# Kernel optimization log

Hardware: AMD Instinct MI355X
Metric: run time of the kernel (lower is better)

## Reference

```python
import jax, jax.numpy as jnp
import numpy as np

B, N, D = 4, 4096, 512
H = 8
HD = D // H  # 64


def setup_inputs() -> dict:
    key = jax.random.key(0)
    ks = jax.random.split(key, 9)
    s = 1.0 / np.sqrt(D)
    return {
        "x": jax.random.normal(ks[0], (B, N, D), dtype=jnp.float32),
        "Wq": jax.random.normal(ks[1], (D, D), dtype=jnp.float32) * s,
        "bq": jax.random.normal(ks[2], (D,), dtype=jnp.float32) * 0.01,
        "Wk": jax.random.normal(ks[3], (D, D), dtype=jnp.float32) * s,
        "bk": jax.random.normal(ks[4], (D,), dtype=jnp.float32) * 0.01,
        "Wv": jax.random.normal(ks[5], (D, D), dtype=jnp.float32) * s,
        "bv": jax.random.normal(ks[6], (D,), dtype=jnp.float32) * 0.01,
        "Wo": jax.random.normal(ks[7], (D, D), dtype=jnp.float32) * s,
        "bo": jax.random.normal(ks[8], (D,), dtype=jnp.float32) * 0.01,
    }


def reference(x, Wq, bq, Wk, bk, Wv, bv, Wo, bo):
    # projections -> [B, H, N, HD]
    def split_heads(t):
        return t.reshape(B, N, H, HD).transpose(0, 2, 1, 3)

    q = split_heads(x @ Wq.T + bq)
    k = split_heads(x @ Wk.T + bk)
    v = split_heads(x @ Wv.T + bv)

    scale = 1.0 / np.sqrt(HD).astype(np.float32)
    scores = jnp.einsum("bhqd,bhkd->bhqk", q, k) * scale  # [B,H,N,N]
    attn = jax.nn.softmax(scores, axis=-1)
    out = jnp.einsum("bhqk,bhkd->bhqd", attn, v)  # [B,H,N,HD]
    out = out.transpose(0, 2, 1, 3).reshape(B, N, D)
    return out @ Wo.T + bo
```

## Files before the change

kernel.cpp:

```cpp
#include <hip/hip_runtime.h>
#include <hip/hip_bf16.h>

#define BB 4
#define NN 4096
#define DD 512
#define HH 8
#define HD 64

typedef __attribute__((ext_vector_type(4))) float f32x4;
typedef __attribute__((ext_vector_type(16))) float f32x16;
typedef __attribute__((ext_vector_type(8))) short short8;
typedef __attribute__((ext_vector_type(4))) unsigned int uint4v;

static __device__ __forceinline__ unsigned short f2bf(float f) {
    unsigned int u = __float_as_uint(f);
    u += 0x7fff + ((u >> 16) & 1);
    return (unsigned short)(u >> 16);
}

__global__ void convert_bf16(const float* __restrict__ in,
                             unsigned short* __restrict__ out, int n) {
    int i = (blockIdx.x * blockDim.x + threadIdx.x) * 8;
    int stride = gridDim.x * blockDim.x * 8;
    for (; i + 7 < n; i += stride) {
        f32x4 a = *reinterpret_cast<const f32x4*>(in + i);
        f32x4 b = *reinterpret_cast<const f32x4*>(in + i + 4);
        short8 o;
        o[0] = (short)f2bf(a[0]); o[1] = (short)f2bf(a[1]);
        o[2] = (short)f2bf(a[2]); o[3] = (short)f2bf(a[3]);
        o[4] = (short)f2bf(b[0]); o[5] = (short)f2bf(b[1]);
        o[6] = (short)f2bf(b[2]); o[7] = (short)f2bf(b[3]);
        *reinterpret_cast<short8*>(out + i) = o;
    }
}

__global__ void convert_weights(const float* __restrict__ W0, const float* __restrict__ W1,
                                const float* __restrict__ W2, const float* __restrict__ W3,
                                unsigned short* __restrict__ out) {
    int which = blockIdx.x >> 7;
    const float* src = which == 0 ? W0 : which == 1 ? W1 : which == 2 ? W2 : W3;
    unsigned short* dst = out + (size_t)which * DD * DD;
    int i = ((blockIdx.x & 127) * blockDim.x + threadIdx.x) * 8;
    f32x4 a = *reinterpret_cast<const f32x4*>(src + i);
    f32x4 b = *reinterpret_cast<const f32x4*>(src + i + 4);
    short8 o;
    o[0] = (short)f2bf(a[0]); o[1] = (short)f2bf(a[1]);
    o[2] = (short)f2bf(a[2]); o[3] = (short)f2bf(a[3]);
    o[4] = (short)f2bf(b[0]); o[5] = (short)f2bf(b[1]);
    o[6] = (short)f2bf(b[2]); o[7] = (short)f2bf(b[3]);
    *reinterpret_cast<short8*>(dst + i) = o;
}

template <int OUT_BF16>
__global__ __launch_bounds__(256)
void gemm_bias(const unsigned short* __restrict__ A,
               const unsigned short* __restrict__ W,
               const float* __restrict__ bias,
               void* __restrict__ Cout, float scale) {
    __shared__ uint4 ldsA[128 * 4];
    __shared__ uint4 ldsB[128 * 4];
    const int t = threadIdx.x;
    const int lane = t & 63;
    const int w = t >> 6;
    const int wr = w >> 1, wc = w & 1;
    const int brow = (int)blockIdx.y * 128;
    const int bcol = (int)blockIdx.x * 128;
    const int l16 = lane & 15;
    const int lq = lane >> 4;

    f32x4 acc[4][4] = {};

    const int sr = t >> 1;
    const int c16 = (t & 1) * 2;

    for (int k0 = 0; k0 < 512; k0 += 32) {
        const uint4* gA = reinterpret_cast<const uint4*>(A + (size_t)(brow + sr) * 512 + k0 + c16 * 8);
        const uint4* gB = reinterpret_cast<const uint4*>(W + (size_t)(bcol + sr) * 512 + k0 + c16 * 8);
        uint4 a0 = gA[0], a1 = gA[1];
        uint4 b0 = gB[0], b1 = gB[1];
        __syncthreads();
        ldsA[(sr * 4 + c16) ^ (sr & 7)]     = a0;
        ldsA[(sr * 4 + c16 + 1) ^ (sr & 7)] = a1;
        ldsB[(sr * 4 + c16) ^ (sr & 7)]     = b0;
        ldsB[(sr * 4 + c16 + 1) ^ (sr & 7)] = b1;
        __syncthreads();
        short8 af[4], bfr[4];
#pragma unroll
        for (int m = 0; m < 4; ++m) {
            int ra = wr * 64 + m * 16 + l16;
            af[m] = *reinterpret_cast<short8*>(&ldsA[(ra * 4 + lq) ^ (ra & 7)]);
            int rb = wc * 64 + m * 16 + l16;
            bfr[m] = *reinterpret_cast<short8*>(&ldsB[(rb * 4 + lq) ^ (rb & 7)]);
        }
#pragma unroll
        for (int m = 0; m < 4; ++m)
#pragma unroll
            for (int n = 0; n < 4; ++n)
                acc[m][n] = __builtin_amdgcn_mfma_f32_16x16x32_bf16(af[m], bfr[n], acc[m][n], 0, 0, 0);
    }

#pragma unroll
    for (int m = 0; m < 4; ++m) {
        int row = brow + wr * 64 + m * 16 + lq * 4;
#pragma unroll
        for (int n = 0; n < 4; ++n) {
            int col = bcol + wc * 64 + n * 16 + l16;
            float bv = bias[col];
#pragma unroll
            for (int r = 0; r < 4; ++r) {
                float v = (acc[m][n][r] + bv) * scale;
                if (OUT_BF16) {
                    ((unsigned short*)Cout)[(size_t)(row + r) * 512 + col] = f2bf(v);
                } else {
                    ((float*)Cout)[(size_t)(row + r) * 512 + col] = v;
                }
            }
        }
    }
}

__global__ __launch_bounds__(256)
void transpose_v(const unsigned short* __restrict__ Vb, unsigned short* __restrict__ Vt) {
    __shared__ unsigned short tile[64][72];
    const int bh = blockIdx.y;
    const int b = bh >> 3, h = bh & 7;
    const int n0 = blockIdx.x * 64;
    const int t = threadIdx.x;
    {
        int r = t >> 2;
        int cs = (t & 3) * 16;
        const short8* src = reinterpret_cast<const short8*>(
            Vb + (size_t)(b * NN + n0 + r) * DD + h * HD + cs);
        short8 v0 = src[0], v1 = src[1];
#pragma unroll
        for (int j = 0; j < 8; ++j) {
            tile[r][cs + j]     = (unsigned short)v0[j];
            tile[r][cs + 8 + j] = (unsigned short)v1[j];
        }
    }
    __syncthreads();
    {
        int d = t >> 2;
        int ns = (t & 3) * 16;
        short8 o0, o1;
#pragma unroll
        for (int j = 0; j < 8; ++j) {
            o0[j] = (short)tile[ns + j][d];
            o1[j] = (short)tile[ns + 8 + j][d];
        }
        unsigned short* dst = Vt + ((size_t)bh * HD + d) * NN + n0 + ns;
        *reinterpret_cast<short8*>(dst)     = o0;
        *reinterpret_cast<short8*>(dst + 8) = o1;
    }
}

__global__ __launch_bounds__(256)
void flash_attn(const unsigned short* __restrict__ Qb,
                const unsigned short* __restrict__ Kb,
                const unsigned short* __restrict__ Vt,
                unsigned short* __restrict__ Ob) {
    __shared__ __align__(16) char lds[32768];
    const int t = threadIdx.x;
    const int lane = t & 63;
    const int w = t >> 6;
    const int nid = (blockIdx.x & 7) * 128 + (blockIdx.x >> 3);
    const int bh = nid >> 5;
    const int qb = nid & 31;
    const int b = bh >> 3, h = bh & 7;
    const int q0 = qb * 128 + w * 32;
    const int l32 = lane & 31;
    const int hi = lane >> 5;

    const int i8 = lane >> 3, g8 = lane & 7;

    const unsigned short* qptr = Qb + (size_t)(b * NN + q0 + l32) * DD + h * HD + hi * 8;
    short8 qf[4];
#pragma unroll
    for (int c = 0; c < 4; ++c)
        qf[c] = *reinterpret_cast<const short8*>(qptr + c * 16);

    short8 ones;
#pragma unroll
    for (int j = 0; j < 8; ++j) ones[j] = (short)0x3F80;

    f32x16 OT0 = {}, OT1 = {}, OTS = {};

    auto STAGE = [&](int kvn, int bb) {
#pragma unroll
        for (int jj = 0; jj < 2; ++jj) {
            int rowl = w * 16 + jj * 8 + i8;
            int gsrc = (g8 ^ i8 ^ ((2 * w + jj) & 7)) * 8;
            const unsigned short* ks = Kb + (size_t)(b * NN + kvn + rowl) * DD + h * HD + gsrc;
            const unsigned short* vs = Vt + ((size_t)bh * HD + rowl) * NN + kvn + gsrc;
            __builtin_amdgcn_global_load_lds(
                (const __attribute__((address_space(1))) void*)ks,
                (__attribute__((address_space(3))) void*)(lds + bb + (w * 16 + jj * 8) * 128),
                16, 0, 0);
            __builtin_amdgcn_global_load_lds(
                (const __attribute__((address_space(1))) void*)vs,
                (__attribute__((address_space(3))) void*)(lds + bb + 8192 + (w * 16 + jj * 8) * 128),
                16, 0, 0);
        }
    };

    STAGE(0, 0);
    __syncthreads();

    int bufb = 0;
    for (int step = 0; step < NN / 64; ++step) {
        if (step < NN / 64 - 1) STAGE((step + 1) * 64, bufb ^ 16384);
        const char* Kt  = lds + bufb;
        const char* Vtl = lds + bufb + 8192;
#pragma unroll
        for (int sub = 0; sub < 2; ++sub) {
            short8 kf[4];
#pragma unroll
            for (int c = 0; c < 4; ++c) {
                int row = sub * 32 + l32;
                int g = (hi + 2 * c) ^ (row & 7) ^ ((row >> 3) & 7);
                kf[c] = *reinterpret_cast<const short8*>(Kt + row * 128 + (g << 4));
            }
            short8 vf[2][2];
#pragma unroll
            for (int dblk = 0; dblk < 2; ++dblk)
#pragma unroll
                for (int c2 = 0; c2 < 2; ++c2) {
                    int row = dblk * 32 + l32;
                    int g = ((sub << 2) + (c2 << 1) + hi) ^ (row & 7) ^ ((row >> 3) & 7);
                    vf[dblk][c2] = *reinterpret_cast<const short8*>(Vtl + row * 128 + (g << 4));
                }
            f32x16 S = {};
            __builtin_amdgcn_s_setprio(1);
            S = __builtin_amdgcn_mfma_f32_32x32x16_bf16(kf[0], qf[0], S, 0, 0, 0);
            S = __builtin_amdgcn_mfma_f32_32x32x16_bf16(kf[1], qf[1], S, 0, 0, 0);
            S = __builtin_amdgcn_mfma_f32_32x32x16_bf16(kf[2], qf[2], S, 0, 0, 0);
            S = __builtin_amdgcn_mfma_f32_32x32x16_bf16(kf[3], qf[3], S, 0, 0, 0);
            __builtin_amdgcn_s_setprio(0);

            unsigned int wq[8];
#pragma unroll
            for (int j = 0; j < 8; ++j) {
                float p0 = __builtin_exp2f(S[2 * j]);
                float p1 = __builtin_exp2f(S[2 * j + 1]);
                asm("v_cvt_pk_bf16_f32 %0, %1, %2" : "=v"(wq[j]) : "v"(p0), "v"(p1));
            }
            asm("v_permlane32_swap_b32 %0, %1" : "+v"(wq[0]), "+v"(wq[2]));
            asm("v_permlane32_swap_b32 %0, %1" : "+v"(wq[1]), "+v"(wq[3]));
            asm("v_permlane32_swap_b32 %0, %1" : "+v"(wq[4]), "+v"(wq[6]));
            asm("v_permlane32_swap_b32 %0, %1" : "+v"(wq[5]), "+v"(wq[7]));
            uint4v pu0 = {wq[0], wq[1], wq[2], wq[3]};
            uint4v pu1 = {wq[4], wq[5], wq[6], wq[7]};
            short8 pc0 = __builtin_bit_cast(short8, pu0);
            short8 pc1 = __builtin_bit_cast(short8, pu1);

            __builtin_amdgcn_s_setprio(1);
            OT0 = __builtin_amdgcn_mfma_f32_32x32x16_bf16(vf[0][0], pc0, OT0, 0, 0, 0);
            OT0 = __builtin_amdgcn_mfma_f32_32x32x16_bf16(vf[0][1], pc1, OT0, 0, 0, 0);
            OT1 = __builtin_amdgcn_mfma_f32_32x32x16_bf16(vf[1][0], pc0, OT1, 0, 0, 0);
            OT1 = __builtin_amdgcn_mfma_f32_32x32x16_bf16(vf[1][1], pc1, OT1, 0, 0, 0);
            OTS = __builtin_amdgcn_mfma_f32_32x32x16_bf16(ones,     pc0, OTS, 0, 0, 0);
            OTS = __builtin_amdgcn_mfma_f32_32x32x16_bf16(ones,     pc1, OTS, 0, 0, 0);
            __builtin_amdgcn_s_setprio(0);
        }
        __syncthreads();
        bufb ^= 16384;
    }

    float inv = 1.0f / OTS[0];
    char* lw = lds + w * 4096;
#pragma unroll
    for (int dblk = 0; dblk < 2; ++dblk) {
#pragma unroll
        for (int g = 0; g < 4; ++g) {
#pragma unroll
            for (int j = 0; j < 2; ++j) {
                int r = 4 * g + 2 * j;
                int d = dblk * 32 + 8 * g + 2 * j + 4 * hi;
                float a = (dblk ? OT1[r] : OT0[r]) * inv;
                float bqv = (dblk ? OT1[r + 1] : OT0[r + 1]) * inv;
                unsigned int wv;
                asm("v_cvt_pk_bf16_f32 %0, %1, %2" : "=v"(wv) : "v"(a), "v"(bqv));
                int addr = (l32 * 128 + d * 2) ^ ((l32 & 7) << 4);
                *reinterpret_cast<unsigned int*>(lw + addr) = wv;
            }
        }
    }
#pragma unroll
    for (int it = 0; it < 4; ++it) {
        int q = lane >> 1;
        int seg = (lane & 1) + it * 2;
        uint4 val = *reinterpret_cast<uint4*>(lw + ((q * 128 + seg * 16) ^ ((q & 7) << 4)));
        *reinterpret_cast<uint4*>(Ob + (size_t)(b * NN + q0 + q) * DD + h * HD + seg * 8) = val;
    }
}

extern "C" void kernel_launch(void* const* d_in, const int* in_sizes, int n_in,
                              void* d_out, int out_size, void* d_ws, size_t ws_size,
                              hipStream_t stream) {
    (void)in_sizes; (void)n_in; (void)out_size; (void)ws_size;
    const float* x  = (const float*)d_in[0];
    const float* Wq = (const float*)d_in[1];
    const float* bq = (const float*)d_in[2];
    const float* Wk = (const float*)d_in[3];
    const float* bk = (const float*)d_in[4];
    const float* Wv = (const float*)d_in[5];
    const float* bv = (const float*)d_in[6];
    const float* Wo = (const float*)d_in[7];
    const float* bo = (const float*)d_in[8];
    float* out = (float*)d_out;

    char* ws = (char*)d_ws;
    const size_t BUF = 16777216;
    unsigned short* xb  = (unsigned short*)(ws);
    unsigned short* Qb  = (unsigned short*)(ws + BUF);
    unsigned short* Kb  = (unsigned short*)(ws + 2 * BUF);
    unsigned short* Vb  = (unsigned short*)(ws + 3 * BUF);
    unsigned short* Wqb = (unsigned short*)(ws + 4 * BUF);
    unsigned short* Wkb = Wqb + 262144;
    unsigned short* Wvb = Wkb + 262144;
    unsigned short* Wob = Wvb + 262144;
    unsigned short* Vt  = xb;
    unsigned short* Ob  = Vb;

    const int NTOK = BB * NN;
    const float cl = 0.125f * 1.4426950408889634f;

    convert_bf16<<<2048, 256, 0, stream>>>(x, xb, NTOK * DD);
    convert_weights<<<512, 256, 0, stream>>>(Wq, Wk, Wv, Wo, Wqb);

    dim3 ggrid(4, NTOK / 128);
    gemm_bias<1><<<ggrid, 256, 0, stream>>>(xb, Wqb, bq, Qb, cl);
    gemm_bias<1><<<ggrid, 256, 0, stream>>>(xb, Wkb, bk, Kb, 1.0f);
    gemm_bias<1><<<ggrid, 256, 0, stream>>>(xb, Wvb, bv, Vb, 1.0f);

    transpose_v<<<dim3(NN / 64, BB * HH), 256, 0, stream>>>(Vb, Vt);

    flash_attn<<<1024, 256, 0, stream>>>(Qb, Kb, Vt, Ob);

    gemm_bias<0><<<ggrid, 256, 0, stream>>>(Ob, Wob, bo, out, 1.0f);
}
```

Measured before the change: 315.8 us.

## Restructure attention inner loop: precompute LDS offsets, interleave two S tiles

Precomputes the swizzled LDS read offsets and the global staging pointers once, and advances the pointers incrementally instead of recomputing addresses every step. The kv loop is unrolled by two so the double-buffer offsets become compile-time constants. Both 32-key S tiles are computed with interleaved MFMA chains, which gives independent MFMAs to hide dependency latency and overlaps the second softmax with PV MFMAs. The setprio hints are dropped, and the extra live fragments raise register pressure.

```diff
diff --git a/kernel.cpp b/kernel.cpp
--- a/kernel.cpp
+++ b/kernel.cpp
@@ -183,87 +183,118 @@
 #pragma unroll
     for (int j = 0; j < 8; ++j) ones[j] = (short)0x3F80;
 
+    const f32x16 Z = {};
     f32x16 OT0 = {}, OT1 = {}, OTS = {};
 
-    auto STAGE = [&](int kvn, int bb) {
-#pragma unroll
-        for (int jj = 0; jj < 2; ++jj) {
-            int rowl = w * 16 + jj * 8 + i8;
-            int gsrc = (g8 ^ i8 ^ ((2 * w + jj) & 7)) * 8;
-            const unsigned short* ks = Kb + (size_t)(b * NN + kvn + rowl) * DD + h * HD + gsrc;
-            const unsigned short* vs = Vt + ((size_t)bh * HD + rowl) * NN + kvn + gsrc;
-            __builtin_amdgcn_global_load_lds(
-                (const __attribute__((address_space(1))) void*)ks,
-                (__attribute__((address_space(3))) void*)(lds + bb + (w * 16 + jj * 8) * 128),
-                16, 0, 0);
-            __builtin_amdgcn_global_load_lds(
-                (const __attribute__((address_space(1))) void*)vs,
-                (__attribute__((address_space(3))) void*)(lds + bb + 8192 + (w * 16 + jj * 8) * 128),
-                16, 0, 0);
-        }
+    int koff[8], voff[8];
+#pragma unroll
+    for (int sub = 0; sub < 2; ++sub) {
+#pragma unroll
+        for (int c = 0; c < 4; ++c) {
+            int row = sub * 32 + l32;
+            int g = (hi + 2 * c) ^ (row & 7) ^ ((row >> 3) & 7);
+            koff[sub * 4 + c] = row * 128 + g * 16;
+        }
+#pragma unroll
+        for (int dblk = 0; dblk < 2; ++dblk)
+#pragma unroll
+            for (int c2 = 0; c2 < 2; ++c2) {
+                int row = dblk * 32 + l32;
+                int g = ((sub << 2) + (c2 << 1) + hi) ^ (row & 7) ^ ((row >> 3) & 7);
+                voff[sub * 4 + dblk * 2 + c2] = 8192 + row * 128 + g * 16;
+            }
+    }
+
+    const int rowl0 = w * 16 + i8;
+    const int rowl1 = w * 16 + 8 + i8;
+    const int gs0 = (g8 ^ i8 ^ ((2 * w) & 7)) * 8;
+    const int gs1 = (g8 ^ i8 ^ ((2 * w + 1) & 7)) * 8;
+    const unsigned short* kp0 = Kb + (size_t)(b * NN + rowl0) * DD + h * HD + gs0;
+    const unsigned short* kp1 = Kb + (size_t)(b * NN + rowl1) * DD + h * HD + gs1;
+    const unsigned short* vp0 = Vt + ((size_t)bh * HD + rowl0) * NN + gs0;
+    const unsigned short* vp1 = Vt + ((size_t)bh * HD + rowl1) * NN + gs1;
+
+    auto STAGE = [&](int bb) {
+        __builtin_amdgcn_global_load_lds(
+            (const __attribute__((address_space(1))) void*)kp0,
+            (__attribute__((address_space(3))) void*)(lds + bb + (w * 16) * 128), 16, 0, 0);
+        __builtin_amdgcn_global_load_lds(
+            (const __attribute__((address_space(1))) void*)kp1,
+            (__attribute__((address_space(3))) void*)(lds + bb + (w * 16 + 8) * 128), 16, 0, 0);
+        __builtin_amdgcn_global_load_lds(
+            (const __attribute__((address_space(1))) void*)vp0,
+            (__attribute__((address_space(3))) void*)(lds + bb + 8192 + (w * 16) * 128), 16, 0, 0);
+        __builtin_amdgcn_global_load_lds(
+            (const __attribute__((address_space(1))) void*)vp1,
+            (__attribute__((address_space(3))) void*)(lds + bb + 8192 + (w * 16 + 8) * 128), 16, 0, 0);
+        kp0 += 64 * DD; kp1 += 64 * DD; vp0 += 64; vp1 += 64;
     };
 
-    STAGE(0, 0);
+    auto softpack = [&](const f32x16& S, short8& pa, short8& pb) {
+        unsigned int wq[8];
+#pragma unroll
+        for (int j = 0; j < 8; ++j) {
+            float p0 = __builtin_exp2f(S[2 * j]);
+            float p1 = __builtin_exp2f(S[2 * j + 1]);
+            asm("v_cvt_pk_bf16_f32 %0, %1, %2" : "=v"(wq[j]) : "v"(p0), "v"(p1));
+        }
+        asm("v_permlane32_swap_b32 %0, %1" : "+v"(wq[0]), "+v"(wq[2]));
+        asm("v_permlane32_swap_b32 %0, %1" : "+v"(wq[1]), "+v"(wq[3]));
+        asm("v_permlane32_swap_b32 %0, %1" : "+v"(wq[4]), "+v"(wq[6]));
+        asm("v_permlane32_swap_b32 %0, %1" : "+v"(wq[5]), "+v"(wq[7]));
+        uint4v pu0 = {wq[0], wq[1], wq[2], wq[3]};
+        uint4v pu1 = {wq[4], wq[5], wq[6], wq[7]};
+        pa = __builtin_bit_cast(short8, pu0);
+        pb = __builtin_bit_cast(short8, pu1);
+    };
+
+    STAGE(0);
     __syncthreads();
 
-    int bufb = 0;
-    for (int step = 0; step < NN / 64; ++step) {
-        if (step < NN / 64 - 1) STAGE((step + 1) * 64, bufb ^ 16384);
-        const char* Kt  = lds + bufb;
-        const char* Vtl = lds + bufb + 8192;
-#pragma unroll
-        for (int sub = 0; sub < 2; ++sub) {
-            short8 kf[4];
-#pragma unroll
-            for (int c = 0; c < 4; ++c) {
-                int row = sub * 32 + l32;
-                int g = (hi + 2 * c) ^ (row & 7) ^ ((row >> 3) & 7);
-                kf[c] = *reinterpret_cast<const short8*>(Kt + row * 128 + (g << 4));
-            }
-            short8 vf[2][2];
-#pragma unroll
-            for (int dblk = 0; dblk < 2; ++dblk)
-#pragma unroll
-                for (int c2 = 0; c2 < 2; ++c2) {
-                    int row = dblk * 32 + l32;
-                    int g = ((sub << 2) + (c2 << 1) + hi) ^ (row & 7) ^ ((row >> 3) & 7);
-                    vf[dblk][c2] = *reinterpret_cast<const short8*>(Vtl + row * 128 + (g << 4));
-                }
-            f32x16 S = {};
-            __builtin_amdgcn_s_setprio(1);
-            S = __builtin_amdgcn_mfma_f32_32x32x16_bf16(kf[0], qf[0], S, 0, 0, 0);
-            S = __builtin_amdgcn_mfma_f32_32x32x16_bf16(kf[1], qf[1], S, 0, 0, 0);
-            S = __builtin_amdgcn_mfma_f32_32x32x16_bf16(kf[2], qf[2], S, 0, 0, 0);
-            S = __builtin_amdgcn_mfma_f32_32x32x16_bf16(kf[3], qf[3], S, 0, 0, 0);
-            __builtin_amdgcn_s_setprio(0);
-
-            unsigned int wq[8];
-#pragma unroll
-            for (int j = 0; j < 8; ++j) {
-                float p0 = __builtin_exp2f(S[2 * j]);
-                float p1 = __builtin_exp2f(S[2 * j + 1]);
-                asm("v_cvt_pk_bf16_f32 %0, %1, %2" : "=v"(wq[j]) : "v"(p0), "v"(p1));
-            }
-            asm("v_permlane32_swap_b32 %0, %1" : "+v"(wq[0]), "+v"(wq[2]));
-            asm("v_permlane32_swap_b32 %0, %1" : "+v"(wq[1]), "+v"(wq[3]));
-            asm("v_permlane32_swap_b32 %0, %1" : "+v"(wq[4]), "+v"(wq[6]));
-            asm("v_permlane32_swap_b32 %0, %1" : "+v"(wq[5]), "+v"(wq[7]));
-            uint4v pu0 = {wq[0], wq[1], wq[2], wq[3]};
-            uint4v pu1 = {wq[4], wq[5], wq[6], wq[7]};
-            short8 pc0 = __builtin_bit_cast(short8, pu0);
-            short8 pc1 = __builtin_bit_cast(short8, pu1);
-
-            __builtin_amdgcn_s_setprio(1);
-            OT0 = __builtin_amdgcn_mfma_f32_32x32x16_bf16(vf[0][0], pc0, OT0, 0, 0, 0);
-            OT0 = __builtin_amdgcn_mfma_f32_32x32x16_bf16(vf[0][1], pc1, OT0, 0, 0, 0);
-            OT1 = __builtin_amdgcn_mfma_f32_32x32x16_bf16(vf[1][0], pc0, OT1, 0, 0, 0);
-            OT1 = __builtin_amdgcn_mfma_f32_32x32x16_bf16(vf[1][1], pc1, OT1, 0, 0, 0);
-            OTS = __builtin_amdgcn_mfma_f32_32x32x16_bf16(ones,     pc0, OTS, 0, 0, 0);
-            OTS = __builtin_amdgcn_mfma_f32_32x32x16_bf16(ones,     pc1, OTS, 0, 0, 0);
-            __builtin_amdgcn_s_setprio(0);
-        }
-        __syncthreads();
-        bufb ^= 16384;
+    for (int it = 0; it < 32; ++it) {
+#pragma unroll
+        for (int half = 0; half < 2; ++half) {
+            const int BO = half ? 16384 : 0;
+            if (half == 0 || it != 31) STAGE(half ? 0 : 16384);
+
+            short8 kf[8];
+#pragma unroll
+            for (int i = 0; i < 8; ++i)
+                kf[i] = *reinterpret_cast<const short8*>(lds + BO + koff[i]);
+
+            f32x16 S0, S1;
+            S0 = __builtin_amdgcn_mfma_f32_32x32x16_bf16(kf[0], qf[0], Z, 0, 0, 0);
+            S1 = __builtin_amdgcn_mfma_f32_32x32x16_bf16(kf[4], qf[0], Z, 0, 0, 0);
+            S0 = __builtin_amdgcn_mfma_f32_32x32x16_bf16(kf[1], qf[1], S0, 0, 0, 0);
+            S1 = __builtin_amdgcn_mfma_f32_32x32x16_bf16(kf[5], qf[1], S1, 0, 0, 0);
+            S0 = __builtin_amdgcn_mfma_f32_32x32x16_bf16(kf[2], qf[2], S0, 0, 0, 0);
+            S1 = __builtin_amdgcn_mfma_f32_32x32x16_bf16(kf[6], qf[2], S1, 0, 0, 0);
+            S0 = __builtin_amdgcn_mfma_f32_32x32x16_bf16(kf[3], qf[3], S0, 0, 0, 0);
+            S1 = __builtin_amdgcn_mfma_f32_32x32x16_bf16(kf[7], qf[3], S1, 0, 0, 0);
+
+            short8 vf[8];
+#pragma unroll
+            for (int i = 0; i < 8; ++i)
+                vf[i] = *reinterpret_cast<const short8*>(lds + BO + voff[i]);
+
+            short8 p0a, p0b, p1a, p1b;
+            softpack(S0, p0a, p0b);
+            OT0 = __builtin_amdgcn_mfma_f32_32x32x16_bf16(vf[0], p0a, OT0, 0, 0, 0);
+            OT0 = __builtin_amdgcn_mfma_f32_32x32x16_bf16(vf[1], p0b, OT0, 0, 0, 0);
+            OT1 = __builtin_amdgcn_mfma_f32_32x32x16_bf16(vf[2], p0a, OT1, 0, 0, 0);
+            OT1 = __builtin_amdgcn_mfma_f32_32x32x16_bf16(vf[3], p0b, OT1, 0, 0, 0);
+            OTS = __builtin_amdgcn_mfma_f32_32x32x16_bf16(ones, p0a, OTS, 0, 0, 0);
+            OTS = __builtin_amdgcn_mfma_f32_32x32x16_bf16(ones, p0b, OTS, 0, 0, 0);
+            softpack(S1, p1a, p1b);
+            OT0 = __builtin_amdgcn_mfma_f32_32x32x16_bf16(vf[4], p1a, OT0, 0, 0, 0);
+            OT0 = __builtin_amdgcn_mfma_f32_32x32x16_bf16(vf[5], p1b, OT0, 0, 0, 0);
+            OT1 = __builtin_amdgcn_mfma_f32_32x32x16_bf16(vf[6], p1a, OT1, 0, 0, 0);
+            OT1 = __builtin_amdgcn_mfma_f32_32x32x16_bf16(vf[7], p1b, OT1, 0, 0, 0);
+            OTS = __builtin_amdgcn_mfma_f32_32x32x16_bf16(ones, p1a, OTS, 0, 0, 0);
+            OTS = __builtin_amdgcn_mfma_f32_32x32x16_bf16(ones, p1b, OTS, 0, 0, 0);
+
+            __syncthreads();
+        }
     }
 
     float inv = 1.0f / OTS[0];
```

New measurement: 304.8 us. -3.5%, faster.
